# Kernel optimization log

Hardware: AMD Instinct MI355X
Metric: run time of the kernel (lower is better)

Reference implementation:

```python
import math
import jax, jax.numpy as jnp
import numpy as np

C, B, T, D = 8, 4, 8192, 64
MAX_LEN = 8192
_DELTA = math.log2(MAX_LEN) / max(C - 1, 1)
# lam_c = 1 - 2^{-(c*delta)}; lam_0 == 0 (memoryless channel)
LAMBDAS = jnp.array([1.0 - 2.0 ** (-(c * _DELTA)) for c in range(C)], dtype=jnp.float32)


def setup_inputs() -> dict:
    key = jax.random.key(0)
    k0, k1, k2 = jax.random.split(key, 3)
    return {
        "channels": jax.random.normal(k0, (C, B, T, D), dtype=jnp.float32),
        "gw_fwd": jax.random.normal(k1, (C, D, D), dtype=jnp.float32) * 0.02,
        "gb_fwd": jnp.ones((C, D), dtype=jnp.float32),
        "gw_bwd": jax.random.normal(k2, (C, D, D), dtype=jnp.float32) * 0.02,
        "gb_bwd": jnp.ones((C, D), dtype=jnp.float32),
    }


def _fixed_decay_scan(lam, v):
    """h_t = lam * h_{t-1} + v_t over axis=1 (time); v: [B,T,D], lam scalar.
    For lam==0 this reduces to identity, matching the torch fast path."""
    a = jnp.full_like(v, lam)

    def combine(x, y):
        a1, b1 = x
        a2, b2 = y
        return (a1 * a2, a2 * b1 + b2)

    return jax.lax.associative_scan(combine, (a, v), axis=1)[1]


def _run_direction(channels, W, b):
    # torch Linear: y = x @ W.T + b, W is (out,in) -> einsum 'cbtd,ced->cbte'
    g = jax.nn.sigmoid(jnp.einsum('cbtd,ced->cbte', channels, W) + b[:, None, None, :])
    gated = g * channels
    return jax.vmap(_fixed_decay_scan)(LAMBDAS, gated)  # [C,B,T,D]


def reference(channels, gw_fwd, gb_fwd, gw_bwd, gb_bwd):
    fwd = _run_direction(channels, gw_fwd, gb_fwd)
    rev = channels[:, :, ::-1, :]
    bwd = _run_direction(rev, gw_bwd, gb_bwd)[:, :, ::-1, :]
    return fwd, bwd
```

## Files before the change

### kernel.cpp

```cpp
#include <hip/hip_runtime.h>
#include <cmath>
#include <cstdint>

typedef __attribute__((ext_vector_type(8))) short short8;
typedef __attribute__((ext_vector_type(4))) float f32x4;
typedef __attribute__((ext_vector_type(2))) unsigned int u32x2;

struct Lams { float v[8]; };

#define NC 8
#define NB 4
#define NT 8192
#define ND 64
#define CL 256
#define NK (NT / CL)
#define NSLOT (2 * NC * NB * NK)
#define NWAVE 8
#define LDH 72

__device__ __forceinline__ uint32_t pk2(float lo, float hi) {
    uint32_t r;
    asm("v_cvt_pk_bf16_f32 %0, %1, %2" : "=v"(r) : "v"(lo), "v"(hi));
    return r;
}

__device__ __forceinline__ float bf2f(unsigned short s) {
    return __builtin_bit_cast(float, (uint32_t)s << 16);
}

__global__ __launch_bounds__(512, 4) void k1_fused(
    const float* __restrict__ x, const float* __restrict__ Wf,
    const float* __restrict__ bf, const float* __restrict__ Wb,
    const float* __restrict__ bb, float* __restrict__ out,
    int* __restrict__ flags, float* __restrict__ evals, Lams lams)
{
    __shared__ unsigned short xbuf[CL * LDH];
    __shared__ float ends_lds[NWAVE][ND];
    __shared__ float hprev_lds[ND];

    const int tid  = threadIdx.x;
    const int lane = tid & 63;
    const int w    = tid >> 6;

    int idx = blockIdx.x;
    const int k   = idx & (NK - 1); idx >>= 5;
    const int b   = idx & (NB - 1); idx >>= 2;
    const int c   = idx & (NC - 1); idx >>= 3;
    const int dir = idx;

    const float lam = lams.v[c];
    const float* W    = (dir ? Wb : Wf) + c * ND * ND;
    const float* bias = (dir ? bb : bf) + c * ND;
    const float* xb   = x + (size_t)(c * NB + b) * NT * ND;
    float* ob = out + (size_t)dir * (size_t)(NC*NB*NT*ND)
                    + (size_t)(c * NB + b) * NT * ND;

    const int er = lane & 15;
    const int ks = lane >> 4;

    const int tr0 = k * CL;
    const int r0  = w * 32;

    {
        const int sr = lane >> 4;
        const int sc = (lane & 15) * 4;
        if (dir == 0) {
            const float* p = xb + (size_t)(tr0 + r0 + sr) * ND + sc;
            #pragma unroll
            for (int g = 0; g < 8; ++g) {
                f32x4 v = *reinterpret_cast<const f32x4*>(p + (size_t)g * 4 * ND);
                u32x2 q = { pk2(v[0], v[1]), pk2(v[2], v[3]) };
                *reinterpret_cast<u32x2*>(&xbuf[(r0 + g*4 + sr) * LDH + sc]) = q;
            }
        } else {
            const float* p = xb + (size_t)(NT-1 - (tr0 + r0 + sr)) * ND + sc;
            #pragma unroll
            for (int g = 0; g < 8; ++g) {
                f32x4 v = *reinterpret_cast<const f32x4*>(p - (size_t)g * 4 * ND);
                u32x2 q = { pk2(v[0], v[1]), pk2(v[2], v[3]) };
                *reinterpret_cast<u32x2*>(&xbuf[(r0 + g*4 + sr) * LDH + sc]) = q;
            }
        }
    }

    short8 bfrag[4][2];
    #pragma unroll
    for (int et = 0; et < 4; ++et) {
        const float* wr = W + (et*16 + er) * ND + ks * 8;
        #pragma unroll
        for (int kk = 0; kk < 2; ++kk) {
            f32x4 lo = *reinterpret_cast<const f32x4*>(wr + kk*32);
            f32x4 hi = *reinterpret_cast<const f32x4*>(wr + kk*32 + 4);
            union { short8 s8; uint32_t u[4]; } t;
            t.u[0] = pk2(lo[0], lo[1]); t.u[1] = pk2(lo[2], lo[3]);
            t.u[2] = pk2(hi[0], hi[1]); t.u[3] = pk2(hi[2], hi[3]);
            bfrag[et][kk] = t.s8;
        }
    }
    float bias_r[4];
    #pragma unroll
    for (int et = 0; et < 4; ++et) bias_r[et] = bias[et*16 + er];

    #pragma unroll
    for (int u = 0; u < 2; ++u) {
        const int rl0 = r0 + u*16;
        short8 afrag[2];
        afrag[0] = *reinterpret_cast<const short8*>(&xbuf[(rl0 + er) * LDH + ks * 8]);
        afrag[1] = *reinterpret_cast<const short8*>(&xbuf[(rl0 + er) * LDH + 32 + ks * 8]);
        #pragma unroll
        for (int et = 0; et < 4; ++et) {
            f32x4 acc = {0.f, 0.f, 0.f, 0.f};
            acc = __builtin_amdgcn_mfma_f32_16x16x32_bf16(afrag[0], bfrag[et][0], acc, 0,0,0);
            acc = __builtin_amdgcn_mfma_f32_16x16x32_bf16(afrag[1], bfrag[et][1], acc, 0,0,0);
            const int col = et*16 + er;
            float gated[4];
            #pragma unroll
            for (int r = 0; r < 4; ++r) {
                const int rl = rl0 + ks*4 + r;
                float z  = acc[r] + bias_r[et];
                float g  = __builtin_amdgcn_rcpf(1.0f + __expf(-z));
                float xv = bf2f(xbuf[rl * LDH + col]);
                gated[r] = g * xv;
            }
            uint32_t p01 = pk2(gated[0], gated[1]);
            uint32_t p23 = pk2(gated[2], gated[3]);
            xbuf[(rl0 + ks*4 + 0) * LDH + col] = (unsigned short)(p01 & 0xFFFF);
            xbuf[(rl0 + ks*4 + 1) * LDH + col] = (unsigned short)(p01 >> 16);
            xbuf[(rl0 + ks*4 + 2) * LDH + col] = (unsigned short)(p23 & 0xFFFF);
            xbuf[(rl0 + ks*4 + 3) * LDH + col] = (unsigned short)(p23 >> 16);
        }
    }

    float lam32 = lam*lam; lam32*=lam32; lam32*=lam32; lam32*=lam32; lam32*=lam32;

    {
        float h = 0.f;
        #pragma unroll
        for (int i = 0; i < 32; ++i) {
            const int a = (r0 + i) * LDH + lane;
            float v = bf2f(xbuf[a]);
            h = fmaf(h, lam, v);
            xbuf[a] = (unsigned short)(pk2(h, h) & 0xFFFF);
        }
        ends_lds[w][lane] = h;
    }
    __syncthreads();

    const int slot = blockIdx.x;
    if (w == NWAVE - 1) {
        float carryW = 0.f;
        #pragma unroll
        for (int j = 0; j < NWAVE - 1; ++j)
            carryW = fmaf(carryW, lam32, ends_lds[j][lane]);
        float E = fmaf(carryW, lam32, ends_lds[NWAVE-1][lane]);

        float Hprev = 0.f;
        if (c != 0) {
            __hip_atomic_store(&evals[(size_t)slot * ND + lane], E,
                               __ATOMIC_RELAXED, __HIP_MEMORY_SCOPE_AGENT);
            asm volatile("s_waitcnt vmcnt(0)" ::: "memory");
            if (lane == 0)
                __hip_atomic_store(&flags[slot], 1, __ATOMIC_RELAXED,
                                   __HIP_MEMORY_SCOPE_AGENT);
            if (k != 0) {
                const int base = slot - k;
                if (lane < k) {
                    while (__hip_atomic_load(&flags[base + lane], __ATOMIC_RELAXED,
                                             __HIP_MEMORY_SCOPE_AGENT) == 0)
                        __builtin_amdgcn_s_sleep(8);
                }
                asm volatile("" ::: "memory");
                const float* eb = evals + (size_t)base * ND;
                float l1 = lam32*lam32; l1 *= l1; l1 *= l1;
                float l4 = l1 * l1; l4 *= l4;
                float P = 0.f;
                int j = 0;
                const int rem = k & 3;
                for (; j < rem; ++j)
                    P = fmaf(P, l1, eb[(size_t)j * ND + lane]);
                for (; j < k; j += 4) {
                    float e0 = eb[(size_t)(j+0) * ND + lane];
                    float e1 = eb[(size_t)(j+1) * ND + lane];
                    float e2 = eb[(size_t)(j+2) * ND + lane];
                    float e3 = eb[(size_t)(j+3) * ND + lane];
                    float t = fmaf(fmaf(fmaf(e0, l1, e1), l1, e2), l1, e3);
                    P = fmaf(P, l4, t);
                }
                Hprev = P;
            }
        }
        hprev_lds[lane] = Hprev;
    }
    __syncthreads();

    {
        const int sr = lane >> 4;
        const int dg = lane & 15;
        float carry4[4];
        #pragma unroll
        for (int j2 = 0; j2 < 4; ++j2) {
            const int d = dg*4 + j2;
            float cy = 0.f, pw = 1.f;
            for (int j = 0; j < w; ++j) {
                cy = fmaf(cy, lam32, ends_lds[j][d]);
                pw *= lam32;
            }
            carry4[j2] = fmaf(pw, hprev_lds[d], cy);
        }
        const float lam2 = lam * lam, lam4 = lam2 * lam2;
        float f = lam;
        for (int j = 0; j < sr; ++j) f *= lam;
        if (dir == 0) {
            float* p = ob + (size_t)(tr0 + r0 + sr) * ND + dg*4;
            #pragma unroll
            for (int g = 0; g < 8; ++g) {
                u32x2 hv = *reinterpret_cast<const u32x2*>(
                    &xbuf[(r0 + g*4 + sr) * LDH + dg*4]);
                f32x4 o;
                o[0] = fmaf(f, carry4[0], bf2f((unsigned short)(hv[0] & 0xFFFF)));
                o[1] = fmaf(f, carry4[1], bf2f((unsigned short)(hv[0] >> 16)));
                o[2] = fmaf(f, carry4[2], bf2f((unsigned short)(hv[1] & 0xFFFF)));
                o[3] = fmaf(f, carry4[3], bf2f((unsigned short)(hv[1] >> 16)));
                *reinterpret_cast<f32x4*>(p + (size_t)g * 4 * ND) = o;
                f *= lam4;
            }
        } else {
            float* p = ob + (size_t)(NT-1 - (tr0 + r0 + sr)) * ND + dg*4;
            #pragma unroll
            for (int g = 0; g < 8; ++g) {
                u32x2 hv = *reinterpret_cast<const u32x2*>(
                    &xbuf[(r0 + g*4 + sr) * LDH + dg*4]);
                f32x4 o;
                o[0] = fmaf(f, carry4[0], bf2f((unsigned short)(hv[0] & 0xFFFF)));
                o[1] = fmaf(f, carry4[1], bf2f((unsigned short)(hv[0] >> 16)));
                o[2] = fmaf(f, carry4[2], bf2f((unsigned short)(hv[1] & 0xFFFF)));
                o[3] = fmaf(f, carry4[3], bf2f((unsigned short)(hv[1] >> 16)));
                *reinterpret_cast<f32x4*>(p - (size_t)g * 4 * ND) = o;
                f *= lam4;
            }
        }
    }
}

extern "C" void kernel_launch(void* const* d_in, const int* in_sizes, int n_in,
                              void* d_out, int out_size, void* d_ws, size_t ws_size,
                              hipStream_t stream)
{
    const float* x  = (const float*)d_in[0];
    const float* Wf = (const float*)d_in[1];
    const float* bf = (const float*)d_in[2];
    const float* Wb = (const float*)d_in[3];
    const float* bb = (const float*)d_in[4];
    float* out = (float*)d_out;

    int*   flags = (int*)d_ws;
    float* evals = (float*)((char*)d_ws + 16384);

    Lams lams;
    const double delta = 13.0 / 7.0;
    for (int c = 0; c < 8; ++c)
        lams.v[c] = (float)(1.0 - pow(2.0, -(double)c * delta));

    hipMemsetAsync(flags, 0, NSLOT * 4, stream);

    dim3 grid(NSLOT);
    k1_fused<<<grid, 512, 0, stream>>>(x, Wf, bf, Wb, bb, out, flags, evals, lams);
}
```

Baseline: 85.89 us.

## Halve grid and process two chunks per block in a persistent-style loop

Result: faster. 70.77 us (-17.6%).

```diff
diff --git a/kernel.cpp b/kernel.cpp
--- a/kernel.cpp
+++ b/kernel.cpp
@@ -13,8 +13,10 @@
 #define NT 8192
 #define ND 64
 #define CL 256
-#define NK (NT / CL)
-#define NSLOT (2 * NC * NB * NK)
+#define NCHUNK 32
+#define NKK 16
+#define NBLK (2 * NC * NB * NKK)
+#define NSLOT (2 * NC * NB * NCHUNK)
 #define NWAVE 8
 #define LDH 72
 
@@ -43,9 +45,9 @@
     const int w    = tid >> 6;
 
     int idx = blockIdx.x;
-    const int k   = idx & (NK - 1); idx >>= 5;
-    const int b   = idx & (NB - 1); idx >>= 2;
-    const int c   = idx & (NC - 1); idx >>= 3;
+    const int kk  = idx & (NKK - 1); idx >>= 4;
+    const int b   = idx & (NB - 1);  idx >>= 2;
+    const int c   = idx & (NC - 1);  idx >>= 3;
     const int dir = idx;
 
     const float lam = lams.v[c];
@@ -54,191 +56,196 @@
     const float* xb   = x + (size_t)(c * NB + b) * NT * ND;
     float* ob = out + (size_t)dir * (size_t)(NC*NB*NT*ND)
                     + (size_t)(c * NB + b) * NT * ND;
+    const int seqbase = (int)(blockIdx.x >> 4) * NCHUNK;
 
     const int er = lane & 15;
     const int ks = lane >> 4;
-
-    const int tr0 = k * CL;
-    const int r0  = w * 32;
-
-    {
-        const int sr = lane >> 4;
-        const int sc = (lane & 15) * 4;
-        if (dir == 0) {
-            const float* p = xb + (size_t)(tr0 + r0 + sr) * ND + sc;
-            #pragma unroll
-            for (int g = 0; g < 8; ++g) {
-                f32x4 v = *reinterpret_cast<const f32x4*>(p + (size_t)g * 4 * ND);
-                u32x2 q = { pk2(v[0], v[1]), pk2(v[2], v[3]) };
-                *reinterpret_cast<u32x2*>(&xbuf[(r0 + g*4 + sr) * LDH + sc]) = q;
-            }
-        } else {
-            const float* p = xb + (size_t)(NT-1 - (tr0 + r0 + sr)) * ND + sc;
-            #pragma unroll
-            for (int g = 0; g < 8; ++g) {
-                f32x4 v = *reinterpret_cast<const f32x4*>(p - (size_t)g * 4 * ND);
-                u32x2 q = { pk2(v[0], v[1]), pk2(v[2], v[3]) };
-                *reinterpret_cast<u32x2*>(&xbuf[(r0 + g*4 + sr) * LDH + sc]) = q;
-            }
-        }
-    }
+    const int r0 = w * 32;
 
     short8 bfrag[4][2];
     #pragma unroll
     for (int et = 0; et < 4; ++et) {
         const float* wr = W + (et*16 + er) * ND + ks * 8;
         #pragma unroll
-        for (int kk = 0; kk < 2; ++kk) {
-            f32x4 lo = *reinterpret_cast<const f32x4*>(wr + kk*32);
-            f32x4 hi = *reinterpret_cast<const f32x4*>(wr + kk*32 + 4);
+        for (int kq = 0; kq < 2; ++kq) {
+            f32x4 lo = *reinterpret_cast<const f32x4*>(wr + kq*32);
+            f32x4 hi = *reinterpret_cast<const f32x4*>(wr + kq*32 + 4);
             union { short8 s8; uint32_t u[4]; } t;
             t.u[0] = pk2(lo[0], lo[1]); t.u[1] = pk2(lo[2], lo[3]);
             t.u[2] = pk2(hi[0], hi[1]); t.u[3] = pk2(hi[2], hi[3]);
-            bfrag[et][kk] = t.s8;
+            bfrag[et][kq] = t.s8;
         }
     }
     float bias_r[4];
     #pragma unroll
     for (int et = 0; et < 4; ++et) bias_r[et] = bias[et*16 + er];
 
-    #pragma unroll
-    for (int u = 0; u < 2; ++u) {
-        const int rl0 = r0 + u*16;
-        short8 afrag[2];
-        afrag[0] = *reinterpret_cast<const short8*>(&xbuf[(rl0 + er) * LDH + ks * 8]);
-        afrag[1] = *reinterpret_cast<const short8*>(&xbuf[(rl0 + er) * LDH + 32 + ks * 8]);
+    float lam32 = lam*lam; lam32*=lam32; lam32*=lam32; lam32*=lam32; lam32*=lam32;
+
+    #pragma unroll 1
+    for (int pass = 0; pass < 2; ++pass) {
+        const int g   = kk + NKK * pass;
+        const int tr0 = g * CL;
+
+        {
+            const int sr = lane >> 4;
+            const int sc = (lane & 15) * 4;
+            if (dir == 0) {
+                const float* p = xb + (size_t)(tr0 + r0 + sr) * ND + sc;
+                #pragma unroll
+                for (int q = 0; q < 8; ++q) {
+                    f32x4 v = *reinterpret_cast<const f32x4*>(p + (size_t)q * 4 * ND);
+                    u32x2 u = { pk2(v[0], v[1]), pk2(v[2], v[3]) };
+                    *reinterpret_cast<u32x2*>(&xbuf[(r0 + q*4 + sr) * LDH + sc]) = u;
+                }
+            } else {
+                const float* p = xb + (size_t)(NT-1 - (tr0 + r0 + sr)) * ND + sc;
+                #pragma unroll
+                for (int q = 0; q < 8; ++q) {
+                    f32x4 v = *reinterpret_cast<const f32x4*>(p - (size_t)q * 4 * ND);
+                    u32x2 u = { pk2(v[0], v[1]), pk2(v[2], v[3]) };
+                    *reinterpret_cast<u32x2*>(&xbuf[(r0 + q*4 + sr) * LDH + sc]) = u;
+                }
+            }
+        }
+
         #pragma unroll
-        for (int et = 0; et < 4; ++et) {
-            f32x4 acc = {0.f, 0.f, 0.f, 0.f};
-            acc = __builtin_amdgcn_mfma_f32_16x16x32_bf16(afrag[0], bfrag[et][0], acc, 0,0,0);
-            acc = __builtin_amdgcn_mfma_f32_16x16x32_bf16(afrag[1], bfrag[et][1], acc, 0,0,0);
-            const int col = et*16 + er;
-            float gated[4];
-            #pragma unroll
-            for (int r = 0; r < 4; ++r) {
-                const int rl = rl0 + ks*4 + r;
-                float z  = acc[r] + bias_r[et];
-                float g  = __builtin_amdgcn_rcpf(1.0f + __expf(-z));
-                float xv = bf2f(xbuf[rl * LDH + col]);
-                gated[r] = g * xv;
-            }
-            uint32_t p01 = pk2(gated[0], gated[1]);
-            uint32_t p23 = pk2(gated[2], gated[3]);
-            xbuf[(rl0 + ks*4 + 0) * LDH + col] = (unsigned short)(p01 & 0xFFFF);
-            xbuf[(rl0 + ks*4 + 1) * LDH + col] = (unsigned short)(p01 >> 16);
-            xbuf[(rl0 + ks*4 + 2) * LDH + col] = (unsigned short)(p23 & 0xFFFF);
-            xbuf[(rl0 + ks*4 + 3) * LDH + col] = (unsigned short)(p23 >> 16);
-        }
-    }
-
-    float lam32 = lam*lam; lam32*=lam32; lam32*=lam32; lam32*=lam32; lam32*=lam32;
-
-    {
-        float h = 0.f;
-        #pragma unroll
-        for (int i = 0; i < 32; ++i) {
-            const int a = (r0 + i) * LDH + lane;
-            float v = bf2f(xbuf[a]);
-            h = fmaf(h, lam, v);
-            xbuf[a] = (unsigned short)(pk2(h, h) & 0xFFFF);
-        }
-        ends_lds[w][lane] = h;
-    }
-    __syncthreads();
-
-    const int slot = blockIdx.x;
-    if (w == NWAVE - 1) {
-        float carryW = 0.f;
-        #pragma unroll
-        for (int j = 0; j < NWAVE - 1; ++j)
-            carryW = fmaf(carryW, lam32, ends_lds[j][lane]);
-        float E = fmaf(carryW, lam32, ends_lds[NWAVE-1][lane]);
-
-        float Hprev = 0.f;
-        if (c != 0) {
-            __hip_atomic_store(&evals[(size_t)slot * ND + lane], E,
-                               __ATOMIC_RELAXED, __HIP_MEMORY_SCOPE_AGENT);
-            asm volatile("s_waitcnt vmcnt(0)" ::: "memory");
-            if (lane == 0)
-                __hip_atomic_store(&flags[slot], 1, __ATOMIC_RELAXED,
-                                   __HIP_MEMORY_SCOPE_AGENT);
-            if (k != 0) {
-                const int base = slot - k;
-                if (lane < k) {
-                    while (__hip_atomic_load(&flags[base + lane], __ATOMIC_RELAXED,
-                                             __HIP_MEMORY_SCOPE_AGENT) == 0)
-                        __builtin_amdgcn_s_sleep(8);
-                }
-                asm volatile("" ::: "memory");
-                const float* eb = evals + (size_t)base * ND;
-                float l1 = lam32*lam32; l1 *= l1; l1 *= l1;
-                float l4 = l1 * l1; l4 *= l4;
-                float P = 0.f;
-                int j = 0;
-                const int rem = k & 3;
-                for (; j < rem; ++j)
-                    P = fmaf(P, l1, eb[(size_t)j * ND + lane]);
-                for (; j < k; j += 4) {
-                    float e0 = eb[(size_t)(j+0) * ND + lane];
-                    float e1 = eb[(size_t)(j+1) * ND + lane];
-                    float e2 = eb[(size_t)(j+2) * ND + lane];
-                    float e3 = eb[(size_t)(j+3) * ND + lane];
-                    float t = fmaf(fmaf(fmaf(e0, l1, e1), l1, e2), l1, e3);
-                    P = fmaf(P, l4, t);
-                }
-                Hprev = P;
-            }
-        }
-        hprev_lds[lane] = Hprev;
-    }
-    __syncthreads();
-
-    {
-        const int sr = lane >> 4;
-        const int dg = lane & 15;
-        float carry4[4];
-        #pragma unroll
-        for (int j2 = 0; j2 < 4; ++j2) {
-            const int d = dg*4 + j2;
-            float cy = 0.f, pw = 1.f;
-            for (int j = 0; j < w; ++j) {
-                cy = fmaf(cy, lam32, ends_lds[j][d]);
-                pw *= lam32;
-            }
-            carry4[j2] = fmaf(pw, hprev_lds[d], cy);
-        }
-        const float lam2 = lam * lam, lam4 = lam2 * lam2;
-        float f = lam;
-        for (int j = 0; j < sr; ++j) f *= lam;
-        if (dir == 0) {
-            float* p = ob + (size_t)(tr0 + r0 + sr) * ND + dg*4;
-            #pragma unroll
-            for (int g = 0; g < 8; ++g) {
-                u32x2 hv = *reinterpret_cast<const u32x2*>(
-                    &xbuf[(r0 + g*4 + sr) * LDH + dg*4]);
-                f32x4 o;
-                o[0] = fmaf(f, carry4[0], bf2f((unsigned short)(hv[0] & 0xFFFF)));
-                o[1] = fmaf(f, carry4[1], bf2f((unsigned short)(hv[0] >> 16)));
-                o[2] = fmaf(f, carry4[2], bf2f((unsigned short)(hv[1] & 0xFFFF)));
-                o[3] = fmaf(f, carry4[3], bf2f((unsigned short)(hv[1] >> 16)));
-                *reinterpret_cast<f32x4*>(p + (size_t)g * 4 * ND) = o;
-                f *= lam4;
-            }
-        } else {
-            float* p = ob + (size_t)(NT-1 - (tr0 + r0 + sr)) * ND + dg*4;
-            #pragma unroll
-            for (int g = 0; g < 8; ++g) {
-                u32x2 hv = *reinterpret_cast<const u32x2*>(
-                    &xbuf[(r0 + g*4 + sr) * LDH + dg*4]);
-                f32x4 o;
-                o[0] = fmaf(f, carry4[0], bf2f((unsigned short)(hv[0] & 0xFFFF)));
-                o[1] = fmaf(f, carry4[1], bf2f((unsigned short)(hv[0] >> 16)));
-                o[2] = fmaf(f, carry4[2], bf2f((unsigned short)(hv[1] & 0xFFFF)));
-                o[3] = fmaf(f, carry4[3], bf2f((unsigned short)(hv[1] >> 16)));
-                *reinterpret_cast<f32x4*>(p - (size_t)g * 4 * ND) = o;
-                f *= lam4;
-            }
-        }
+        for (int u = 0; u < 2; ++u) {
+            const int rl0 = r0 + u*16;
+            short8 afrag[2];
+            afrag[0] = *reinterpret_cast<const short8*>(&xbuf[(rl0 + er) * LDH + ks * 8]);
+            afrag[1] = *reinterpret_cast<const short8*>(&xbuf[(rl0 + er) * LDH + 32 + ks * 8]);
+            #pragma unroll
+            for (int et = 0; et < 4; ++et) {
+                f32x4 acc = {0.f, 0.f, 0.f, 0.f};
+                acc = __builtin_amdgcn_mfma_f32_16x16x32_bf16(afrag[0], bfrag[et][0], acc, 0,0,0);
+                acc = __builtin_amdgcn_mfma_f32_16x16x32_bf16(afrag[1], bfrag[et][1], acc, 0,0,0);
+                const int col = et*16 + er;
+                float gated[4];
+                #pragma unroll
+                for (int r = 0; r < 4; ++r) {
+                    const int rl = rl0 + ks*4 + r;
+                    float z  = acc[r] + bias_r[et];
+                    float gg = __builtin_amdgcn_rcpf(1.0f + __expf(-z));
+                    float xv = bf2f(xbuf[rl * LDH + col]);
+                    gated[r] = gg * xv;
+                }
+                uint32_t p01 = pk2(gated[0], gated[1]);
+                uint32_t p23 = pk2(gated[2], gated[3]);
+                xbuf[(rl0 + ks*4 + 0) * LDH + col] = (unsigned short)(p01 & 0xFFFF);
+                xbuf[(rl0 + ks*4 + 1) * LDH + col] = (unsigned short)(p01 >> 16);
+                xbuf[(rl0 + ks*4 + 2) * LDH + col] = (unsigned short)(p23 & 0xFFFF);
+                xbuf[(rl0 + ks*4 + 3) * LDH + col] = (unsigned short)(p23 >> 16);
+            }
+        }
+
+        {
+            float h = 0.f;
+            #pragma unroll
+            for (int i = 0; i < 32; ++i) {
+                const int a = (r0 + i) * LDH + lane;
+                float v = bf2f(xbuf[a]);
+                h = fmaf(h, lam, v);
+                xbuf[a] = (unsigned short)(pk2(h, h) & 0xFFFF);
+            }
+            ends_lds[w][lane] = h;
+        }
+        __syncthreads();
+
+        if (w == NWAVE - 1) {
+            float carryW = 0.f;
+            #pragma unroll
+            for (int j = 0; j < NWAVE - 1; ++j)
+                carryW = fmaf(carryW, lam32, ends_lds[j][lane]);
+            float E = fmaf(carryW, lam32, ends_lds[NWAVE-1][lane]);
+
+            float Hprev = 0.f;
+            if (c != 0) {
+                const int slot = seqbase + g;
+                __hip_atomic_store(&evals[(size_t)slot * ND + lane], E,
+                                   __ATOMIC_RELAXED, __HIP_MEMORY_SCOPE_AGENT);
+                asm volatile("s_waitcnt vmcnt(0)" ::: "memory");
+                if (lane == 0)
+                    __hip_atomic_store(&flags[slot], 1, __ATOMIC_RELAXED,
+                                       __HIP_MEMORY_SCOPE_AGENT);
+                if (g != 0) {
+                    if (lane < g) {
+                        while (__hip_atomic_load(&flags[seqbase + lane], __ATOMIC_RELAXED,
+                                                 __HIP_MEMORY_SCOPE_AGENT) == 0)
+                            __builtin_amdgcn_s_sleep(8);
+                    }
+                    asm volatile("" ::: "memory");
+                    const float* eb = evals + (size_t)seqbase * ND;
+                    float l1 = lam32*lam32; l1 *= l1; l1 *= l1;
+                    float l4 = l1 * l1; l4 *= l4;
+                    float P = 0.f;
+                    int j = 0;
+                    const int rem = g & 3;
+                    for (; j < rem; ++j)
+                        P = fmaf(P, l1, eb[(size_t)j * ND + lane]);
+                    for (; j < g; j += 4) {
+                        float e0 = eb[(size_t)(j+0) * ND + lane];
+                        float e1 = eb[(size_t)(j+1) * ND + lane];
+                        float e2 = eb[(size_t)(j+2) * ND + lane];
+                        float e3 = eb[(size_t)(j+3) * ND + lane];
+                        float t = fmaf(fmaf(fmaf(e0, l1, e1), l1, e2), l1, e3);
+                        P = fmaf(P, l4, t);
+                    }
+                    Hprev = P;
+                }
+            }
+            hprev_lds[lane] = Hprev;
+        }
+        __syncthreads();
+
+        {
+            const int sr = lane >> 4;
+            const int dg = lane & 15;
+            float carry4[4];
+            #pragma unroll
+            for (int j2 = 0; j2 < 4; ++j2) {
+                const int d = dg*4 + j2;
+                float cy = 0.f, pw = 1.f;
+                for (int j = 0; j < w; ++j) {
+                    cy = fmaf(cy, lam32, ends_lds[j][d]);
+                    pw *= lam32;
+                }
+                carry4[j2] = fmaf(pw, hprev_lds[d], cy);
+            }
+            const float lam2 = lam * lam, lam4 = lam2 * lam2;
+            float f = lam;
+            for (int j = 0; j < sr; ++j) f *= lam;
+            if (dir == 0) {
+                float* p = ob + (size_t)(tr0 + r0 + sr) * ND + dg*4;
+                #pragma unroll
+                for (int q = 0; q < 8; ++q) {
+                    u32x2 hv = *reinterpret_cast<const u32x2*>(
+                        &xbuf[(r0 + q*4 + sr) * LDH + dg*4]);
+                    f32x4 o;
+                    o[0] = fmaf(f, carry4[0], bf2f((unsigned short)(hv[0] & 0xFFFF)));
+                    o[1] = fmaf(f, carry4[1], bf2f((unsigned short)(hv[0] >> 16)));
+                    o[2] = fmaf(f, carry4[2], bf2f((unsigned short)(hv[1] & 0xFFFF)));
+                    o[3] = fmaf(f, carry4[3], bf2f((unsigned short)(hv[1] >> 16)));
+                    *reinterpret_cast<f32x4*>(p + (size_t)q * 4 * ND) = o;
+                    f *= lam4;
+                }
+            } else {
+                float* p = ob + (size_t)(NT-1 - (tr0 + r0 + sr)) * ND + dg*4;
+                #pragma unroll
+                for (int q = 0; q < 8; ++q) {
+                    u32x2 hv = *reinterpret_cast<const u32x2*>(
+                        &xbuf[(r0 + q*4 + sr) * LDH + dg*4]);
+                    f32x4 o;
+                    o[0] = fmaf(f, carry4[0], bf2f((unsigned short)(hv[0] & 0xFFFF)));
+                    o[1] = fmaf(f, carry4[1], bf2f((unsigned short)(hv[0] >> 16)));
+                    o[2] = fmaf(f, carry4[2], bf2f((unsigned short)(hv[1] & 0xFFFF)));
+                    o[3] = fmaf(f, carry4[3], bf2f((unsigned short)(hv[1] >> 16)));
+                    *reinterpret_cast<f32x4*>(p - (size_t)q * 4 * ND) = o;
+                    f *= lam4;
+                }
+            }
+        }
+        __syncthreads();
     }
 }
 
@@ -263,6 +270,6 @@
 
     hipMemsetAsync(flags, 0, NSLOT * 4, stream);
 
-    dim3 grid(NSLOT);
+    dim3 grid(NBLK);
     k1_fused<<<grid, 512, 0, stream>>>(x, Wf, bf, Wb, bb, out, flags, evals, lams);
 }
```
